# Performance work log

Hardware: AMD Instinct MI355X
Metric: run time of the kernel (lower is better)

Reference implementation:

```python
import jax, jax.numpy as jnp
import numpy as np

B, L, E, H = 4, 2048, 1024, 16
D = E // H  # per-head dim

def setup_inputs() -> dict:
    key = jax.random.key(0)
    ks = jax.random.split(key, 12)
    xav = lambda k, shape: jax.random.normal(k, shape, jnp.float32) * (2.0 / (shape[0] + shape[-1])) ** 0.5
    embeddings = jax.random.normal(ks[0], (B, L, E), jnp.float32)
    pre_proj_w = xav(ks[1], (E, E)); pre_proj_b = jnp.zeros((E,), jnp.float32)
    pre_sparse_w = xav(ks[2], (E, E)); pre_sparse_b = jnp.zeros((E,), jnp.float32)
    toeplitz_psfs = xav(ks[3], (H, 2 * L - 1, D))
    post_conv_w = xav(ks[4], (E, E)); post_conv_b = jnp.zeros((E,), jnp.float32)
    dens = 0.01
    num_nz = int(L * L * dens)
    idxs = jax.random.randint(ks[5], (num_nz, 2), 0, L)
    vals = jnp.abs(jax.random.normal(ks[6], (num_nz,), jnp.float32))
    sparse = jnp.zeros((L, L), jnp.float32).at[idxs[:, 0], idxs[:, 1]].add(vals)
    ln_gamma = jnp.ones((E,), jnp.float32); ln_beta = jnp.zeros((E,), jnp.float32)
    return {"embeddings": embeddings, "pre_proj_w": pre_proj_w, "pre_proj_b": pre_proj_b,
            "pre_sparse_w": pre_sparse_w, "pre_sparse_b": pre_sparse_b,
            "toeplitz_psfs": toeplitz_psfs, "post_conv_w": post_conv_w, "post_conv_b": post_conv_b,
            "sparse": sparse, "ln_gamma": ln_gamma, "ln_beta": ln_beta}

def reference(embeddings, pre_proj_w, pre_proj_b, pre_sparse_w, pre_sparse_b,
              toeplitz_psfs, post_conv_w, post_conv_b, sparse, ln_gamma, ln_beta):
    b, l, e = embeddings.shape
    h, two_l_m1, d = toeplitz_psfs.shape
    # causal PSF mask: first l taps kept, trailing l-1 zeroed (before softmax)
    psf_mask = jnp.concatenate([jnp.ones((l,)), jnp.zeros((l - 1,))])[None, :, None]
    psfs = jax.nn.softmax(toeplitz_psfs * psf_mask, axis=1)  # softmax over 2l-1 taps
    # pre-projection
    pre = jnp.einsum('ble,oe->blo', embeddings, pre_proj_w) + pre_proj_b
    # pad seq to 2l-1 and split heads: [b, h, 2l-1, d]
    padded = jnp.pad(pre, ((0, 0), (0, l - 1), (0, 0)))
    padded = padded.reshape(b, two_l_m1, h, d).transpose(0, 2, 1, 3)
    # 2D FFT convolution over (seq, per-head-dim)
    psf_fft = jnp.fft.fftn(psfs, axes=(1, 2))              # [h, 2l-1, d]
    emb_fft = jnp.fft.fftn(padded, axes=(2, 3))            # [b, h, 2l-1, d]
    conv = jnp.real(jnp.fft.ifftn(psf_fft[None] * emb_fft, axes=(2, 3)))[:, :, :l, :]
    conv = jax.nn.gelu(conv, approximate=False)
    conv = conv.transpose(0, 2, 1, 3).reshape(b, l, e)
    conv_emb = jnp.einsum('ble,oe->blo', conv, post_conv_w) + post_conv_b
    # sparse branch (causal lower-triangular mask)
    sparse_masked = sparse * jnp.tril(jnp.ones((l, l), sparse.dtype))
    pre_sparse = jnp.einsum('ble,oe->blo', pre, pre_sparse_w) + pre_sparse_b
    sparse_emb = jnp.einsum('ls,bse->ble', sparse_masked, pre_sparse)
    # residual + layernorm (dropout = identity at eval)
    x = conv_emb + sparse_emb + embeddings
    mu = jnp.mean(x, axis=-1, keepdims=True)
    var = jnp.mean(jnp.square(x - mu), axis=-1, keepdims=True)
    return (x - mu) * jax.lax.rsqrt(var + 1e-12) * ln_gamma + ln_beta
```

## Files before the change

### kernel.cpp

```cpp
#include <hip/hip_runtime.h>
#include <hip/hip_bf16.h>
#include <hip/hip_fp16.h>
#include <math.h>

#define B_ 4
#define L_ 2048
#define E_ 1024
#define H_ 16
#define D_ 64
#define NFFT 4096
#define CAP 128

typedef __hip_bfloat16 bf16;
typedef __attribute__((ext_vector_type(8))) short bf16x8;
typedef __attribute__((ext_vector_type(4))) float f32x4;
typedef __attribute__((ext_vector_type(2))) __fp16 f16x2;

typedef __attribute__((address_space(1))) const unsigned int gas_u32;
typedef __attribute__((address_space(3))) unsigned int las_u32;

__device__ __forceinline__ void gload_lds16(const void* g, void* l) {
    __builtin_amdgcn_global_load_lds((gas_u32*)g, (las_u32*)l, 16, 0, 0);
}

#define SL(i) ((i) + ((i) >> 4))
#define LDSN (NFFT + NFFT / 16)

__device__ __forceinline__ float bfu2f(unsigned short u) {
    return __uint_as_float(((unsigned)u) << 16);
}
__device__ __forceinline__ f16x2 pk2(float a, float b) {
    return __builtin_amdgcn_cvt_pkrtz(a, b);
}

__device__ __forceinline__ int drev64(int k) {
    return ((k & 3) << 4) | (k & 12) | ((k >> 4) & 3);
}

#define C1R 0.923879532511287f
#define C1I -0.382683432365090f
#define C2R 0.707106781186548f
#define C2I -0.707106781186548f
#define C3R 0.382683432365090f
#define C3I -0.923879532511287f

__device__ __forceinline__ void r4dif_w(float& x0r, float& x0i, float& x1r, float& x1i,
                                        float& x2r, float& x2i, float& x3r, float& x3i,
                                        float w1r, float w1i) {
    float a0r = x0r + x2r, a0i = x0i + x2i, a1r = x0r - x2r, a1i = x0i - x2i;
    float a2r = x1r + x3r, a2i = x1i + x3i, a3r = x1r - x3r, a3i = x1i - x3i;
    float y0r = a0r + a2r, y0i = a0i + a2i, y2r = a0r - a2r, y2i = a0i - a2i;
    float y1r = a1r + a3i, y1i = a1i - a3r, y3r = a1r - a3i, y3i = a1i + a3r;
    float w2r = w1r * w1r - w1i * w1i, w2i = 2.0f * w1r * w1i;
    float w3r = w2r * w1r - w2i * w1i, w3i = w2r * w1i + w2i * w1r;
    x0r = y0r; x0i = y0i;
    x1r = y1r * w1r - y1i * w1i; x1i = y1r * w1i + y1i * w1r;
    x2r = y2r * w2r - y2i * w2i; x2i = y2r * w2i + y2i * w2r;
    x3r = y3r * w3r - y3i * w3i; x3i = y3r * w3i + y3i * w3r;
}
__device__ __forceinline__ void r4dif_nt(float& x0r, float& x0i, float& x1r, float& x1i,
                                         float& x2r, float& x2i, float& x3r, float& x3i) {
    float a0r = x0r + x2r, a0i = x0i + x2i, a1r = x0r - x2r, a1i = x0i - x2i;
    float a2r = x1r + x3r, a2i = x1i + x3i, a3r = x1r - x3r, a3i = x1i - x3i;
    x0r = a0r + a2r; x0i = a0i + a2i;
    x2r = a0r - a2r; x2i = a0i - a2i;
    float y1r = a1r + a3i, y1i = a1i - a3r, y3r = a1r - a3i, y3i = a1i + a3r;
    x1r = y1r; x1i = y1i; x3r = y3r; x3i = y3i;
}
__device__ __forceinline__ void r4dit_w(float& x0r, float& x0i, float& x1r, float& x1i,
                                        float& x2r, float& x2i, float& x3r, float& x3i,
                                        float w1r, float w1i) {
    float w2r = w1r * w1r - w1i * w1i, w2i = 2.0f * w1r * w1i;
    float w3r = w2r * w1r - w2i * w1i, w3i = w2r * w1i + w2i * w1r;
    float z1r = x1r * w1r + x1i * w1i, z1i = x1i * w1r - x1r * w1i;
    float z2r = x2r * w2r + x2i * w2i, z2i = x2i * w2r - x2r * w2i;
    float z3r = x3r * w3r + x3i * w3i, z3i = x3i * w3r - x3r * w3i;
    float b0r = x0r + z2r, b0i = x0i + z2i, b1r = x0r - z2r, b1i = x0i - z2i;
    float b2r = z1r + z3r, b2i = z1i + z3i, b3r = z1r - z3r, b3i = z1i - z3i;
    x0r = b0r + b2r; x0i = b0i + b2i;
    x2r = b0r - b2r; x2i = b0i - b2i;
    x1r = b1r - b3i; x1i = b1i + b3r;
    x3r = b1r + b3i; x3i = b1i - b3r;
}
__device__ __forceinline__ void r4dit_nt(float& x0r, float& x0i, float& x1r, float& x1i,
                                         float& x2r, float& x2i, float& x3r, float& x3i) {
    float b0r = x0r + x2r, b0i = x0i + x2i, b1r = x0r - x2r, b1i = x0i - x2i;
    float b2r = x1r + x3r, b2i = x1i + x3i, b3r = x1r - x3r, b3i = x1i - x3i;
    x0r = b0r + b2r; x0i = b0i + b2i;
    x2r = b0r - b2r; x2i = b0i - b2i;
    x1r = b1r - b3i; x1i = b1i + b3r;
    x3r = b1r + b3i; x3i = b1i - b3r;
}

__device__ __forceinline__ void fftA_fwd(float* xr, float* xi, float wpr, float wpi) {
    r4dif_w(xr[0], xi[0], xr[4], xi[4], xr[8], xi[8], xr[12], xi[12], wpr, wpi);
    r4dif_w(xr[1], xi[1], xr[5], xi[5], xr[9], xi[9], xr[13], xi[13],
            wpr * C1R - wpi * C1I, wpr * C1I + wpi * C1R);
    r4dif_w(xr[2], xi[2], xr[6], xi[6], xr[10], xi[10], xr[14], xi[14],
            wpr * C2R - wpi * C2I, wpr * C2I + wpi * C2R);
    r4dif_w(xr[3], xi[3], xr[7], xi[7], xr[11], xi[11], xr[15], xi[15],
            wpr * C3R - wpi * C3I, wpr * C3I + wpi * C3R);
    float s2r = wpr * wpr - wpi * wpi, s2i = 2.0f * wpr * wpi;
    float w4r = s2r * s2r - s2i * s2i, w4i = 2.0f * s2r * s2i;
#pragma unroll
    for (int g = 0; g < 4; ++g)
        r4dif_w(xr[4 * g], xi[4 * g], xr[4 * g + 1], xi[4 * g + 1], xr[4 * g + 2],
                xi[4 * g + 2], xr[4 * g + 3], xi[4 * g + 3], w4r, w4i);
}
__device__ __forceinline__ void fftA_inv(float* xr, float* xi, float wpr, float wpi) {
    float s2r = wpr * wpr - wpi * wpi, s2i = 2.0f * wpr * wpi;
    float w4r = s2r * s2r - s2i * s2i, w4i = 2.0f * s2r * s2i;
#pragma unroll
    for (int g = 0; g < 4; ++g)
        r4dit_w(xr[4 * g], xi[4 * g], xr[4 * g + 1], xi[4 * g + 1], xr[4 * g + 2],
                xi[4 * g + 2], xr[4 * g + 3], xi[4 * g + 3], w4r, w4i);
    r4dit_w(xr[0], xi[0], xr[4], xi[4], xr[8], xi[8], xr[12], xi[12], wpr, wpi);
    r4dit_w(xr[1], xi[1], xr[5], xi[5], xr[9], xi[9], xr[13], xi[13],
            wpr * C1R - wpi * C1I, wpr * C1I + wpi * C1R);
    r4dit_w(xr[2], xi[2], xr[6], xi[6], xr[10], xi[10], xr[14], xi[14],
            wpr * C2R - wpi * C2I, wpr * C2I + wpi * C2R);
    r4dit_w(xr[3], xi[3], xr[7], xi[7], xr[11], xi[11], xr[15], xi[15],
            wpr * C3R - wpi * C3I, wpr * C3I + wpi * C3R);
}
__device__ __forceinline__ void fftB_fwd(float* xr, float* xi, float wor, float woi) {
    r4dif_w(xr[0], xi[0], xr[4], xi[4], xr[8], xi[8], xr[12], xi[12], wor, woi);
    r4dif_w(xr[1], xi[1], xr[5], xi[5], xr[9], xi[9], xr[13], xi[13],
            wor * C1R - woi * C1I, wor * C1I + woi * C1R);
    r4dif_w(xr[2], xi[2], xr[6], xi[6], xr[10], xi[10], xr[14], xi[14],
            wor * C2R - woi * C2I, wor * C2I + woi * C2R);
    r4dif_w(xr[3], xi[3], xr[7], xi[7], xr[11], xi[11], xr[15], xi[15],
            wor * C3R - woi * C3I, wor * C3I + woi * C3R);
    float s2r = wor * wor - woi * woi, s2i = 2.0f * wor * woi;
    float w4r = s2r * s2r - s2i * s2i, w4i = 2.0f * s2r * s2i;
#pragma unroll
    for (int g = 0; g < 4; ++g)
        r4dif_w(xr[4 * g], xi[4 * g], xr[4 * g + 1], xi[4 * g + 1], xr[4 * g + 2],
                xi[4 * g + 2], xr[4 * g + 3], xi[4 * g + 3], w4r, w4i);
}
__device__ __forceinline__ void fftB_inv(float* xr, float* xi, float wor, float woi) {
    float s2r = wor * wor - woi * woi, s2i = 2.0f * wor * woi;
    float w4r = s2r * s2r - s2i * s2i, w4i = 2.0f * s2r * s2i;
#pragma unroll
    for (int g = 0; g < 4; ++g)
        r4dit_w(xr[4 * g], xi[4 * g], xr[4 * g + 1], xi[4 * g + 1], xr[4 * g + 2],
                xi[4 * g + 2], xr[4 * g + 3], xi[4 * g + 3], w4r, w4i);
    r4dit_w(xr[0], xi[0], xr[4], xi[4], xr[8], xi[8], xr[12], xi[12], wor, woi);
    r4dit_w(xr[1], xi[1], xr[5], xi[5], xr[9], xi[9], xr[13], xi[13],
            wor * C1R - woi * C1I, wor * C1I + woi * C1R);
    r4dit_w(xr[2], xi[2], xr[6], xi[6], xr[10], xi[10], xr[14], xi[14],
            wor * C2R - woi * C2I, wor * C2I + woi * C2R);
    r4dit_w(xr[3], xi[3], xr[7], xi[7], xr[11], xi[11], xr[15], xi[15],
            wor * C3R - woi * C3I, wor * C3I + woi * C3R);
}
__device__ __forceinline__ void fftC_fwd(float* xr, float* xi) {
    r4dif_w(xr[0], xi[0], xr[4], xi[4], xr[8], xi[8], xr[12], xi[12], 1.0f, 0.0f);
    r4dif_w(xr[1], xi[1], xr[5], xi[5], xr[9], xi[9], xr[13], xi[13], C1R, C1I);
    r4dif_w(xr[2], xi[2], xr[6], xi[6], xr[10], xi[10], xr[14], xi[14], C2R, C2I);
    r4dif_w(xr[3], xi[3], xr[7], xi[7], xr[11], xi[11], xr[15], xi[15], C3R, C3I);
#pragma unroll
    for (int g = 0; g < 4; ++g)
        r4dif_nt(xr[4 * g], xi[4 * g], xr[4 * g + 1], xi[4 * g + 1], xr[4 * g + 2],
                 xi[4 * g + 2], xr[4 * g + 3], xi[4 * g + 3]);
}
__device__ __forceinline__ void fftC_inv(float* xr, float* xi) {
#pragma unroll
    for (int g = 0; g < 4; ++g)
        r4dit_nt(xr[4 * g], xi[4 * g], xr[4 * g + 1], xi[4 * g + 1], xr[4 * g + 2],
                 xi[4 * g + 2], xr[4 * g + 3], xi[4 * g + 3]);
    r4dit_w(xr[0], xi[0], xr[4], xi[4], xr[8], xi[8], xr[12], xi[12], 1.0f, 0.0f);
    r4dit_w(xr[1], xi[1], xr[5], xi[5], xr[9], xi[9], xr[13], xi[13], C1R, C1I);
    r4dit_w(xr[2], xi[2], xr[6], xi[6], xr[10], xi[10], xr[14], xi[14], C2R, C2I);
    r4dit_w(xr[3], xi[3], xr[7], xi[7], xr[11], xi[11], xr[15], xi[15], C3R, C3I);
}

template <int CONJ>
__device__ inline void fft64_rows(float* xr, float* xi, int tid,
                                  const float2* __restrict__ tw) {
    for (int st = 0; st < 3; ++st) {
        int q = 1 << (4 - 2 * st);
        __syncthreads();
        for (int it = 0; it < 4; ++it) {
            int w = tid + (it << 8);
            int lc = w & 63, bc = w >> 6;
            int p = bc & (q - 1);
            int basev = ((bc & ~(q - 1)) << 2) | p;
            int i0 = basev * 66 + lc, i1 = i0 + q * 66, i2 = i1 + q * 66, i3 = i2 + q * 66;
            float x0r = xr[i0], x0i = xi[i0], x1r = xr[i1], x1i = xi[i1];
            float x2r = xr[i2], x2i = xi[i2], x3r = xr[i3], x3i = xi[i3];
            float a0r = x0r + x2r, a0i = x0i + x2i;
            float a1r = x0r - x2r, a1i = x0i - x2i;
            float a2r = x1r + x3r, a2i = x1i + x3i;
            float a3r = x1r - x3r, a3i = x1i - x3i;
            float y0r = a0r + a2r, y0i = a0i + a2i;
            float y2r = a0r - a2r, y2i = a0i - a2i;
            float y1r, y1i, y3r, y3i;
            if (!CONJ) {
                y1r = a1r + a3i; y1i = a1i - a3r;
                y3r = a1r - a3i; y3i = a1i + a3r;
            } else {
                y1r = a1r - a3i; y1i = a1i + a3r;
                y3r = a1r + a3i; y3i = a1i - a3r;
            }
            int e = (p << (2 * st)) * 64;
            float2 w1 = tw[e];
            float w1x = w1.x, w1y = CONJ ? -w1.y : w1.y;
            float w2x = w1x * w1x - w1y * w1y, w2y = 2.0f * w1x * w1y;
            float w3x = w2x * w1x - w2y * w1y, w3y = w2x * w1y + w2y * w1x;
            xr[i0] = y0r; xi[i0] = y0i;
            xr[i1] = y1r * w1x - y1i * w1y; xi[i1] = y1r * w1y + y1i * w1x;
            xr[i2] = y2r * w2x - y2i * w2y; xi[i2] = y2r * w2y + y2i * w2x;
            xr[i3] = y3r * w3x - y3i * w3y; xi[i3] = y3r * w3y + y3i * w3x;
        }
    }
    __syncthreads();
}

__device__ inline void fft64_b(float* xr, float* xi, int tid,
                               const float2* __restrict__ tw) {
    for (int st = 0; st < 3; ++st) {
        int q = 1 << (4 - 2 * st);
        __syncthreads();
        for (int it = 0; it < 4; ++it) {
            int b = tid + (it << 8);
            int fc = b & 63;
            int bc = b >> 6;
            int p = bc & (q - 1);
            int basev = ((bc & ~(q - 1)) << 2) | p;
            int i0 = basev * 64 + fc, i1 = i0 + q * 64, i2 = i1 + q * 64, i3 = i2 + q * 64;
            float x0r = xr[i0], x0i = xi[i0], x1r = xr[i1], x1i = xi[i1];
            float x2r = xr[i2], x2i = xi[i2], x3r = xr[i3], x3i = xi[i3];
            float a0r = x0r + x2r, a0i = x0i + x2i;
            float a1r = x0r - x2r, a1i = x0i - x2i;
            float a2r = x1r + x3r, a2i = x1i + x3i;
            float a3r = x1r - x3r, a3i = x1i - x3i;
            float y0r = a0r + a2r, y0i = a0i + a2i;
            float y2r = a0r - a2r, y2i = a0i - a2i;
            float y1r = a1r + a3i, y1i = a1i - a3r;
            float y3r = a1r - a3i, y3i = a1i + a3r;
            int e = (p << (2 * st)) * 64;
            float2 w1 = tw[e];
            float w2x = w1.x * w1.x - w1.y * w1.y, w2y = 2.0f * w1.x * w1.y;
            float w3x = w2x * w1.x - w2y * w1.y, w3y = w2x * w1.y + w2y * w1.x;
            xr[i0] = y0r; xi[i0] = y0i;
            xr[i1] = y1r * w1.x - y1i * w1.y; xi[i1] = y1r * w1.y + y1i * w1.x;
            xr[i2] = y2r * w2x - y2i * w2y; xi[i2] = y2r * w2y + y2i * w2x;
            xr[i3] = y3r * w3x - y3i * w3y; xi[i3] = y3r * w3y + y3i * w3x;
        }
    }
    __syncthreads();
}

#define NB_TW 16
#define NB_CVT 8192
#define NB_CVTW 3072
#define NB_TF 512
#define NB_SP 2048
__global__ __launch_bounds__(256) void k_prologue(const float* __restrict__ emb,
                                                  const float* __restrict__ W1,
                                                  const float* __restrict__ W2,
                                                  const float* __restrict__ W3,
                                                  const float* __restrict__ psfs,
                                                  const float* __restrict__ Sp,
                                                  float2* __restrict__ tw,
                                                  bf16* __restrict__ embb,
                                                  bf16* __restrict__ Wb,
                                                  float* __restrict__ psfT,
                                                  int* __restrict__ nnz,
                                                  int* __restrict__ idxs,
                                                  float* __restrict__ vals) {
    __shared__ float tile[64][65];
    __shared__ int cnt;
    int tid = threadIdx.x;
    int blk = blockIdx.x;
    if (blk < NB_TW) {
        int k = blk * 256 + tid;
        float ang = -(float)k * (float)(M_PI / 2048.0);
        tw[k] = make_float2(cosf(ang), sinf(ang));
        return;
    }
    blk -= NB_TW;
    if (blk < NB_CVT) {
        int i = (blk * 256 + tid) * 4;
        float4 v = *(const float4*)(emb + i);
        bf16 tmp[4];
        tmp[0] = __float2bfloat16(v.x); tmp[1] = __float2bfloat16(v.y);
        tmp[2] = __float2bfloat16(v.z); tmp[3] = __float2bfloat16(v.w);
        *(ushort4*)(embb + i) = *(ushort4*)tmp;
        return;
    }
    blk -= NB_CVT;
    if (blk < NB_CVTW) {
        int w = blk >> 10;
        const float* src = (w == 0) ? W1 : (w == 1) ? W2 : W3;
        int i = ((blk & 1023) * 256 + tid) * 4;
        float4 v = *(const float4*)(src + i);
        bf16 tmp[4];
        tmp[0] = __float2bfloat16(v.x); tmp[1] = __float2bfloat16(v.y);
        tmp[2] = __float2bfloat16(v.z); tmp[3] = __float2bfloat16(v.w);
        *(ushort4*)(Wb + (size_t)w * E_ * E_ + i) = *(ushort4*)tmp;
        return;
    }
    blk -= NB_CVTW;
    if (blk < NB_TF) {
        int z = blk >> 5;
        int r0 = (blk & 31) * 64;
        const float* in = psfs + (size_t)z * (2 * L_ - 1) * D_;
        float* out = psfT + (size_t)z * D_ * L_;
        int tx4 = (tid & 15) * 4, ty = tid >> 4;
#pragma unroll
        for (int k = 0; k < 4; ++k) {
            int r = ty + 16 * k;
            float4 v = *(const float4*)&in[(size_t)(r0 + r) * D_ + tx4];
            tile[r][tx4 + 0] = v.x; tile[r][tx4 + 1] = v.y;
            tile[r][tx4 + 2] = v.z; tile[r][tx4 + 3] = v.w;
        }
        __syncthreads();
#pragma unroll
        for (int k = 0; k < 4; ++k) {
            int c = ty + 16 * k;
            float4 w;
            w.x = tile[tx4 + 0][c]; w.y = tile[tx4 + 1][c];
            w.z = tile[tx4 + 2][c]; w.w = tile[tx4 + 3][c];
            *(float4*)&out[(size_t)c * L_ + r0 + tx4] = w;
        }
        return;
    }
    blk -= NB_TF;
    {
        int l = blk;
        if (tid == 0) cnt = 0;
        __syncthreads();
        const float* row = Sp + (size_t)l * L_;
        for (int s = tid; s <= l; s += 256) {
            float v = row[s];
            if (v != 0.0f) {
                int slot = atomicAdd(&cnt, 1);
                if (slot < CAP) { idxs[l * CAP + slot] = s; vals[l * CAP + slot] = v; }
            }
        }
        __syncthreads();
        if (tid == 0) nnz[l] = min(cnt, CAP);
    }
}

template <int OUTB>
__global__ __launch_bounds__(256) void k_gemm_mfma(const bf16* __restrict__ A,
                                                   const bf16* __restrict__ Wt,
                                                   const float* __restrict__ bias,
                                                   float* __restrict__ C,
                                                   bf16* __restrict__ Cb,
                                                   int M, int N, int K) {
    __shared__ bf16 As[64 * 64];
    __shared__ bf16 Bs[128 * 64];
    int tid = threadIdx.x;
    int lane = tid & 63, w = tid >> 6;
    int wr = w >> 1, wc = w & 1;

    int nwg = gridDim.x * gridDim.y;
    int flat = blockIdx.y * gridDim.x + blockIdx.x;
    int cpx = nwg >> 3;
    int swz = (flat & 7) * cpx + (flat >> 3);
    int bx = (swz % gridDim.x) * 128;
    int by = (swz / gridDim.x) * 64;

    f32x4 zz = {0.0f, 0.0f, 0.0f, 0.0f};
    f32x4 acc[2][4];
#pragma unroll
    for (int m = 0; m < 2; ++m)
#pragma unroll
        for (int n = 0; n < 4; ++n) acc[m][n] = zz;

    int koff = (lane >> 4) * 8;
    int rsub = lane & 15;

    for (int k0 = 0; k0 < K; k0 += 64) {
#pragma unroll
        for (int i = 0; i < 2; ++i) {
            int c = tid + i * 256;
            int row = c >> 3;
            int kb = (c & 7) * 8;
            int kbs = kb ^ ((row & 7) << 3);
            gload_lds16(A + (size_t)(by + row) * K + k0 + kbs, &As[c * 8]);
        }
#pragma unroll
        for (int i = 0; i < 4; ++i) {
            int c = tid + i * 256;
            int row = c >> 3;
            int kb = (c & 7) * 8;
            int kbs = kb ^ ((row & 7) << 3);
            gload_lds16(Wt + (size_t)(bx + row) * K + k0 + kbs, &Bs[c * 8]);
        }
        __syncthreads();
#pragma unroll
        for (int half = 0; half < 2; ++half) {
            int ko = koff + half * 32;
            bf16x8 af[2], bfv[4];
#pragma unroll
            for (int m = 0; m < 2; ++m) {
                int R = wr * 32 + m * 16 + rsub;
                af[m] = *(const bf16x8*)&As[R * 64 + (ko ^ ((R & 7) << 3))];
            }
#pragma unroll
            for (int n = 0; n < 4; ++n) {
                int R = wc * 64 + n * 16 + rsub;
                bfv[n] = *(const bf16x8*)&Bs[R * 64 + (ko ^ ((R & 7) << 3))];
            }
#pragma unroll
            for (int m = 0; m < 2; ++m)
#pragma unroll
                for (int n = 0; n < 4; ++n)
                    acc[m][n] = __builtin_amdgcn_mfma_f32_16x16x32_bf16(af[m], bfv[n], acc[m][n], 0, 0, 0);
        }
        __syncthreads();
    }

    int cq = (lane >> 4) * 4;
    int cr = lane & 15;
#pragma unroll
    for (int m = 0; m < 2; ++m) {
        int row0 = by + wr * 32 + m * 16 + cq;
#pragma unroll
        for (int n = 0; n < 4; ++n) {
            int col = bx + wc * 64 + n * 16 + cr;
            float bv = bias[col];
#pragma unroll
            for (int j = 0; j < 4; ++j) {
                float v = acc[m][n][j] + bv;
                if constexpr (OUTB)
                    Cb[(size_t)(row0 + j) * N + col] = __float2bfloat16(v);
                else
                    C[(size_t)(row0 + j) * N + col] = v;
            }
        }
    }
}

__global__ __launch_bounds__(256) void k_build_khat(const float* __restrict__ psfT,
                                                    f16x2* __restrict__ Khat,
                                                    const float2* __restrict__ tw) {
    __shared__ f16x2 fl[LDSN];
    __shared__ float red[256];
    int u = blockIdx.x, h = blockIdx.y, tid = threadIdx.x;
    const float* col = psfT + ((size_t)(h * D_ + u)) * L_;
    int p = tid;

    float2 twp = tw[p];
    float2 two = tw[(tid & 15) * 16];

    float v[8];
#pragma unroll
    for (int j = 0; j < 8; ++j) v[j] = col[p + 256 * j];

    float lm = v[0];
#pragma unroll
    for (int j = 1; j < 8; ++j) lm = fmaxf(lm, v[j]);
    red[tid] = lm; __syncthreads();
    for (int off = 128; off > 0; off >>= 1) {
        if (tid < off) red[tid] = fmaxf(red[tid], red[tid + off]);
        __syncthreads();
    }
    float M = fmaxf(red[0], 0.0f);
    __syncthreads();

    float e[8];
    float ls = 0.0f;
#pragma unroll
    for (int j = 0; j < 8; ++j) { e[j] = expf(v[j] - M); ls += e[j]; }
    red[tid] = ls; __syncthreads();
    for (int off = 128; off > 0; off >>= 1) {
        if (tid < off) red[tid] += red[tid + off];
        __syncthreads();
    }
    float Z = red[0] + (float)(L_ - 1) * expf(-M);
    float invZ = 1.0f / Z;
    float cval = expf(-M) * invZ;

    float xr[16], xi[16];
#pragma unroll
    for (int j = 0; j < 16; ++j) {
        int i = p + 256 * j;
        xr[j] = (j < 8) ? e[j] * invZ : ((i == 2048) ? 0.0f : cval);
        xi[j] = 0.0f;
    }
    __syncthreads();

    fftA_fwd(xr, xi, twp.x, twp.y);
#pragma unroll
    for (int j = 0; j < 16; ++j) fl[SL(p + 256 * j)] = pk2(xr[j], xi[j]);
    __syncthreads();
    {
        int bb = tid >> 4, o = tid & 15;
#pragma unroll
        for (int j = 0; j < 16; ++j) {
            f16x2 hh = fl[SL(bb * 256 + o + 16 * j)];
            xr[j] = (float)hh.x; xi[j] = (float)hh.y;
        }
        fftB_fwd(xr, xi, two.x, two.y);
#pragma unroll
        for (int j = 0; j < 16; ++j)
            fl[SL(bb * 256 + o + 16 * j)] = pk2(xr[j], xi[j]);
    }
    __syncthreads();
#pragma unroll
    for (int j = 0; j < 16; ++j) {
        f16x2 hh = fl[SL(16 * tid + j)];
        xr[j] = (float)hh.x; xi[j] = (float)hh.y;
    }
    fftC_fwd(xr, xi);

    float sc = 1.0f / (float)NFFT;
    f16x2* outp = Khat + ((size_t)h * D_ + u) * NFFT + 16 * tid;
#pragma unroll
    for (int j = 0; j < 16; ++j) outp[j] = pk2(xr[j] * sc, xi[j] * sc);
}

__global__ __launch_bounds__(256) void k_dfft_vfft(f16x2* __restrict__ Khat,
                                                   const bf16* __restrict__ preb,
                                                   f16x2* __restrict__ Xv,
                                                   const float2* __restrict__ tw) {
    __shared__ float smem[2 * 4224];
    float* Xre = smem;
    float* Xim = smem + 4224;
    int tid = threadIdx.x;
    int blk = blockIdx.x;
    if (blk < 1024) {
        int f0 = (blk & 63) * 64, h = blk >> 6;
        f16x2* kb = Khat + (size_t)h * D_ * NFFT;
        for (int i = tid; i < 4096; i += 256) {
            int uu = i >> 6, fc = i & 63;
            f16x2 v = kb[(size_t)uu * NFFT + f0 + fc];
            Xre[i] = (float)v.x; Xim[i] = (float)v.y;
        }
        fft64_b(Xre, Xim, tid, tw);
        float sc = 1.0f / 64.0f;
        for (int i = tid; i < 4096; i += 256) {
            int s = i >> 6, fc = i & 63;
            kb[(size_t)drev64(s) * NFFT + f0 + fc] = pk2(Xre[i] * sc, Xim[i] * sc);
        }
        return;
    }
    blk -= 1024;
    {
        int l0 = (blk & 31) * 64, h = (blk >> 5) & 15, b = blk >> 9;
        const bf16* src = preb + ((size_t)(b * L_ + l0)) * E_ + h * 64;
#pragma unroll
        for (int it = 0; it < 2; ++it) {
            int c = tid + it * 256;
            int lc = c >> 3, v8 = (c & 7) * 8;
            bf16x8 xv8 = *(const bf16x8*)(src + (size_t)lc * E_ + v8);
#pragma unroll
            for (int j = 0; j < 8; ++j) {
                Xre[(v8 + j) * 66 + lc] = bfu2f((unsigned short)xv8[j]);
                Xim[(v8 + j) * 66 + lc] = 0.0f;
            }
        }
        fft64_rows<0>(Xre, Xim, tid, tw);
        for (int i = tid; i < 33 * 64; i += 256) {
            int k = i >> 6, lc = i & 63;
            int s = drev64(k);
            Xv[((size_t)(b * H_ + h) * 33 + k) * L_ + l0 + lc] =
                pk2(Xre[s * 66 + lc], Xim[s * 66 + lc]);
        }
    }
}

__global__ __launch_bounds__(256) void k_seqconv(f16x2* __restrict__ Xv,
                                                 const f16x2* __restrict__ Khat,
                                                 const float2* __restrict__ tw) {
    __shared__ f16x2 fl[LDSN];
    int k = blockIdx.x, h = blockIdx.y, b = blockIdx.z;
    int tid = threadIdx.x, p = tid;
    f16x2* col = Xv + ((size_t)(b * H_ + h) * 33 + k) * L_;

    float2 twp = tw[p];
    float2 two = tw[(tid & 15) * 16];

    float xr[16], xi[16];
#pragma unroll
    for (int j = 0; j < 16; ++j) {
        if (j < 8) {
            f16x2 z = col[p + 256 * j];
            xr[j] = (float)z.x; xi[j] = (float)z.y;
        } else { xr[j] = 0.0f; xi[j] = 0.0f; }
    }
    fftA_fwd(xr, xi, twp.x, twp.y);
#pragma unroll
    for (int j = 0; j < 16; ++j) fl[SL(p + 256 * j)] = pk2(xr[j], xi[j]);
    __syncthreads();
    {
        int bb = tid >> 4, o = tid & 15;
#pragma unroll
        for (int j = 0; j < 16; ++j) {
            f16x2 hh = fl[SL(bb * 256 + o + 16 * j)];
            xr[j] = (float)hh.x; xi[j] = (float)hh.y;
        }
        fftB_fwd(xr, xi, two.x, two.y);
#pragma unroll
        for (int j = 0; j < 16; ++j)
            fl[SL(bb * 256 + o + 16 * j)] = pk2(xr[j], xi[j]);
    }
    __syncthreads();
    {
        const f16x2* khp = Khat + ((size_t)h * 64 + k) * NFFT + 16 * tid;
        f16x2 kk[16];
#pragma unroll
        for (int j = 0; j < 16; ++j) kk[j] = khp[j];
#pragma unroll
        for (int j = 0; j < 16; ++j) {
            f16x2 hh = fl[SL(16 * tid + j)];
            xr[j] = (float)hh.x; xi[j] = (float)hh.y;
        }
        fftC_fwd(xr, xi);
#pragma unroll
        for (int j = 0; j < 16; ++j) {
            float kr = (float)kk[j].x, ki = (float)kk[j].y;
            float ar = xr[j], ai = xi[j];
            xr[j] = ar * kr - ai * ki;
            xi[j] = ar * ki + ai * kr;
        }
        fftC_inv(xr, xi);
#pragma unroll
        for (int j = 0; j < 16; ++j) fl[SL(16 * tid + j)] = pk2(xr[j], xi[j]);
    }
    __syncthreads();
    {
        int bb = tid >> 4, o = tid & 15;
#pragma unroll
        for (int j = 0; j < 16; ++j) {
            f16x2 hh = fl[SL(bb * 256 + o + 16 * j)];
            xr[j] = (float)hh.x; xi[j] = (float)hh.y;
        }
        fftB_inv(xr, xi, two.x, two.y);
#pragma unroll
        for (int j = 0; j < 16; ++j)
            fl[SL(bb * 256 + o + 16 * j)] = pk2(xr[j], xi[j]);
    }
    __syncthreads();
#pragma unroll
    for (int j = 0; j < 16; ++j) {
        f16x2 hh = fl[SL(p + 256 * j)];
        xr[j] = (float)hh.x; xi[j] = (float)hh.y;
    }
    fftA_inv(xr, xi, twp.x, twp.y);
#pragma unroll
    for (int j = 0; j < 8; ++j)
        col[p + 256 * j] = pk2(xr[j], xi[j]);
}

__global__ __launch_bounds__(256) void k_vifft(const f16x2* __restrict__ Xv,
                                               bf16* __restrict__ actb,
                                               const float2* __restrict__ tw) {
    __shared__ float Xre[64 * 66];
    __shared__ float Xim[64 * 66];
    int l0 = blockIdx.x * 64, h = blockIdx.y, b = blockIdx.z;
    int tid = threadIdx.x;
    for (int i = tid; i < 33 * 64; i += 256) {
        int k = i >> 6, lc = i & 63;
        f16x2 z = Xv[((size_t)(b * H_ + h) * 33 + k) * L_ + l0 + lc];
        Xre[k * 66 + lc] = (float)z.x; Xim[k * 66 + lc] = (float)z.y;
    }
    __syncthreads();
    for (int i = tid; i < 31 * 64; i += 256) {
        int k = 33 + (i >> 6), lc = i & 63;
        Xre[k * 66 + lc] =  Xre[(64 - k) * 66 + lc];
        Xim[k * 66 + lc] = -Xim[(64 - k) * 66 + lc];
    }
    fft64_rows<1>(Xre, Xim, tid, tw);
    bf16* dst = actb + ((size_t)(b * L_ + l0)) * E_ + h * 64;
#pragma unroll
    for (int it = 0; it < 2; ++it) {
        int c = tid + it * 256;
        int lc = c >> 3, m8 = (c & 7) * 8;
        unsigned short o[8];
#pragma unroll
        for (int j = 0; j < 8; ++j) {
            float x = Xre[drev64(m8 + j) * 66 + lc];
            float g = 0.5f * x * (1.0f + erff(x * 0.70710678118654752f));
            bf16 bb = __float2bfloat16(g);
            o[j] = *(unsigned short*)&bb;
        }
        *(ushort4*)(dst + (size_t)lc * E_ + m8)     = make_ushort4(o[0], o[1], o[2], o[3]);
        *(ushort4*)(dst + (size_t)lc * E_ + m8 + 4) = make_ushort4(o[4], o[5], o[6], o[7]);
    }
}

__global__ __launch_bounds__(256) void k_spmm_ln(const int* __restrict__ nnz,
                                                 const int* __restrict__ idxs,
                                                 const float* __restrict__ vals,
                                                 const bf16* __restrict__ P,
                                                 const bf16* __restrict__ accbb,
                                                 const float* __restrict__ emb,
                                                 const float* __restrict__ gamma,
                                                 const float* __restrict__ beta,
                                                 float* __restrict__ outp) {
    __shared__ int sidx[CAP];
    __shared__ float sval[CAP];
    __shared__ float red[256];
    int l = blockIdx.x, b = blockIdx.y, tid = threadIdx.x;
    int n = nnz[l];
    for (int j = tid; j < n; j += 256) {
        sidx[j] = idxs[l * CAP + j];
        sval[j] = vals[l * CAP + j];
    }
    __syncthreads();
    size_t off = (size_t)tid * 4;
    size_t rowbase = ((size_t)(b * L_ + l)) * E_;
    ushort4 a4 = *(const ushort4*)(accbb + rowbase + off);
    float4 e4 = *(const float4*)(emb + rowbase + off);
    float x0 = bfu2f(a4.x) + e4.x;
    float x1 = bfu2f(a4.y) + e4.y;
    float x2 = bfu2f(a4.z) + e4.z;
    float x3 = bfu2f(a4.w) + e4.w;
    const bf16* Pb = P + (size_t)b * L_ * E_;
    for (int j = 0; j < n; ++j) {
        float v = sval[j];
        ushort4 p = *(const ushort4*)(Pb + (size_t)sidx[j] * E_ + off);
        x0 += v * bfu2f(p.x); x1 += v * bfu2f(p.y);
        x2 += v * bfu2f(p.z); x3 += v * bfu2f(p.w);
    }
    red[tid] = x0 + x1 + x2 + x3; __syncthreads();
    for (int o2 = 128; o2 > 0; o2 >>= 1) {
        if (tid < o2) red[tid] += red[tid + o2];
        __syncthreads();
    }
    float mu = red[0] * (1.0f / E_);
    __syncthreads();
    float d0 = x0 - mu, d1 = x1 - mu, d2 = x2 - mu, d3 = x3 - mu;
    red[tid] = d0 * d0 + d1 * d1 + d2 * d2 + d3 * d3; __syncthreads();
    for (int o2 = 128; o2 > 0; o2 >>= 1) {
        if (tid < o2) red[tid] += red[tid + o2];
        __syncthreads();
    }
    float inv = rsqrtf(red[0] * (1.0f / E_) + 1e-12f);
    float4 g4 = *(const float4*)(gamma + off);
    float4 b4 = *(const float4*)(beta + off);
    float4 o4;
    o4.x = d0 * inv * g4.x + b4.x;
    o4.y = d1 * inv * g4.y + b4.y;
    o4.z = d2 * inv * g4.z + b4.z;
    o4.w = d3 * inv * g4.w + b4.w;
    *(float4*)(outp + rowbase + off) = o4;
}

extern "C" void kernel_launch(void* const* d_in, const int* in_sizes, int n_in,
                              void* d_out, int out_size, void* d_ws, size_t ws_size,
                              hipStream_t stream) {
    const float* emb    = (const float*)d_in[0];
    const float* W1     = (const float*)d_in[1];
    const float* b1     = (const float*)d_in[2];
    const float* W2     = (const float*)d_in[3];
    const float* b2     = (const float*)d_in[4];
    const float* psfs   = (const float*)d_in[5];
    const float* W3     = (const float*)d_in[6];
    const float* b3     = (const float*)d_in[7];
    const float* sparse = (const float*)d_in[8];
    const float* gamma  = (const float*)d_in[9];
    const float* beta   = (const float*)d_in[10];
    float* outp = (float*)d_out;

    const size_t BLE  = (size_t)B_ * L_ * E_;
    const size_t EE   = (size_t)E_ * E_;
    const size_t KSZ  = (size_t)H_ * D_ * NFFT;
    const size_t XVSZ = (size_t)B_ * H_ * 33 * L_;

    bf16*   accbb      = (bf16*)d_ws;
    bf16*   pre_sparse = accbb + BLE;
    f16x2*  Khat       = (f16x2*)(pre_sparse + BLE);
    f16x2*  Xv         = Khat + KSZ;
    bf16*   preb       = (bf16*)(Xv + XVSZ);
    bf16*   actb       = preb + BLE;
    bf16*   W1b        = actb + BLE;
    bf16*   W2b        = W1b + EE;
    bf16*   W3b        = W2b + EE;
    float2* twd        = (float2*)(W3b + EE);
    int*    s_nnz      = (int*)(twd + NFFT);
    int*    s_idx      = s_nnz + L_;
    float*  s_val      = (float*)(s_idx + (size_t)L_ * CAP);
    float*  psfT       = (float*)Xv;

    k_prologue<<<NB_TW + NB_CVT + NB_CVTW + NB_TF + NB_SP, 256, 0, stream>>>(
        emb, W1, W2, W3, psfs, sparse, twd, actb, W1b, psfT, s_nnz, s_idx, s_val);

    k_gemm_mfma<1><<<dim3(E_ / 128, (B_ * L_) / 64), 256, 0, stream>>>(
        actb, W1b, b1, nullptr, preb, B_ * L_, E_, E_);
    k_gemm_mfma<1><<<dim3(E_ / 128, (B_ * L_) / 64), 256, 0, stream>>>(
        preb, W2b, b2, nullptr, pre_sparse, B_ * L_, E_, E_);

    k_build_khat<<<dim3(D_, H_), 256, 0, stream>>>(psfT, Khat, twd);

    k_dfft_vfft<<<1024 + 2048, 256, 0, stream>>>(Khat, preb, Xv, twd);

    k_seqconv<<<dim3(33, H_, B_), 256, 0, stream>>>(Xv, Khat, twd);

    k_vifft<<<dim3(L_ / 64, H_, B_), 256, 0, stream>>>(Xv, actb, twd);

    k_gemm_mfma<1><<<dim3(E_ / 128, (B_ * L_) / 64), 256, 0, stream>>>(
        actb, W3b, b3, nullptr, accbb, B_ * L_, E_, E_);

    k_spmm_ln<<<dim3(L_, B_), 256, 0, stream>>>(
        s_nnz, s_idx, s_val, pre_sparse, accbb, emb, gamma, beta, outp);
}
```

Before: 210.5 us.

## Merge independent GEMM and FFT stages into shared heterogeneous launches

Packs independent work into combined kernels split by block index. The first GEMM now runs alongside the PSF kernel-FFT build, and the second GEMM runs alongside the D-axis FFT of Khat and the value FFT. The goal is to cut launch count and idle tail time by filling the GPU with independent work. The cost is that every block in a merged kernel reserves the largest shared-memory footprint (33 KB), which may lower occupancy for the GEMM blocks.

```diff
diff --git a/kernel.cpp b/kernel.cpp
--- a/kernel.cpp
+++ b/kernel.cpp
@@ -343,25 +343,22 @@
     }
 }
 
-template <int OUTB>
-__global__ __launch_bounds__(256) void k_gemm_mfma(const bf16* __restrict__ A,
-                                                   const bf16* __restrict__ Wt,
-                                                   const float* __restrict__ bias,
-                                                   float* __restrict__ C,
-                                                   bf16* __restrict__ Cb,
-                                                   int M, int N, int K) {
-    __shared__ bf16 As[64 * 64];
-    __shared__ bf16 Bs[128 * 64];
+__device__ __forceinline__ void gemm_body(void* smemraw, int flat, int nwgx,
+                                          const bf16* __restrict__ A,
+                                          const bf16* __restrict__ Wt,
+                                          const float* __restrict__ bias,
+                                          bf16* __restrict__ Cb,
+                                          int nwg, int N, int K) {
+    bf16* As = (bf16*)smemraw;
+    bf16* Bs = As + 64 * 64;
     int tid = threadIdx.x;
     int lane = tid & 63, w = tid >> 6;
     int wr = w >> 1, wc = w & 1;
 
-    int nwg = gridDim.x * gridDim.y;
-    int flat = blockIdx.y * gridDim.x + blockIdx.x;
     int cpx = nwg >> 3;
     int swz = (flat & 7) * cpx + (flat >> 3);
-    int bx = (swz % gridDim.x) * 128;
-    int by = (swz / gridDim.x) * 64;
+    int bx = (swz % nwgx) * 128;
+    int by = (swz / nwgx) * 64;
 
     f32x4 zz = {0.0f, 0.0f, 0.0f, 0.0f};
     f32x4 acc[2][4];
@@ -426,21 +423,20 @@
 #pragma unroll
             for (int j = 0; j < 4; ++j) {
                 float v = acc[m][n][j] + bv;
-                if constexpr (OUTB)
-                    Cb[(size_t)(row0 + j) * N + col] = __float2bfloat16(v);
-                else
-                    C[(size_t)(row0 + j) * N + col] = v;
+                Cb[(size_t)(row0 + j) * N + col] = __float2bfloat16(v);
             }
         }
     }
 }
 
-__global__ __launch_bounds__(256) void k_build_khat(const float* __restrict__ psfT,
-                                                    f16x2* __restrict__ Khat,
-                                                    const float2* __restrict__ tw) {
-    __shared__ f16x2 fl[LDSN];
-    __shared__ float red[256];
-    int u = blockIdx.x, h = blockIdx.y, tid = threadIdx.x;
+__device__ __forceinline__ void khat_body(void* smemraw, int blk,
+                                          const float* __restrict__ psfT,
+                                          f16x2* __restrict__ Khat,
+                                          const float2* __restrict__ tw) {
+    f16x2* fl = (f16x2*)smemraw;
+    float* red = (float*)(fl + LDSN);
+    int u = blk & 63, h = blk >> 6;
+    int tid = threadIdx.x;
     const float* col = psfT + ((size_t)(h * D_ + u)) * L_;
     int p = tid;
 
@@ -514,54 +510,94 @@
     for (int j = 0; j < 16; ++j) outp[j] = pk2(xr[j] * sc, xi[j] * sc);
 }
 
-__global__ __launch_bounds__(256) void k_dfft_vfft(f16x2* __restrict__ Khat,
-                                                   const bf16* __restrict__ preb,
-                                                   f16x2* __restrict__ Xv,
-                                                   const float2* __restrict__ tw) {
-    __shared__ float smem[2 * 4224];
-    float* Xre = smem;
-    float* Xim = smem + 4224;
+__device__ __forceinline__ void dfft_body(void* smemraw, int blk,
+                                          f16x2* __restrict__ Khat,
+                                          const float2* __restrict__ tw) {
+    float* Xre = (float*)smemraw;
+    float* Xim = Xre + 4224;
     int tid = threadIdx.x;
+    int f0 = (blk & 63) * 64, h = blk >> 6;
+    f16x2* kb = Khat + (size_t)h * D_ * NFFT;
+    for (int i = tid; i < 4096; i += 256) {
+        int uu = i >> 6, fc = i & 63;
+        f16x2 v = kb[(size_t)uu * NFFT + f0 + fc];
+        Xre[i] = (float)v.x; Xim[i] = (float)v.y;
+    }
+    fft64_b(Xre, Xim, tid, tw);
+    float sc = 1.0f / 64.0f;
+    for (int i = tid; i < 4096; i += 256) {
+        int s = i >> 6, fc = i & 63;
+        kb[(size_t)drev64(s) * NFFT + f0 + fc] = pk2(Xre[i] * sc, Xim[i] * sc);
+    }
+}
+
+__device__ __forceinline__ void vfft_body(void* smemraw, int blk,
+                                          const bf16* __restrict__ preb,
+                                          f16x2* __restrict__ Xv,
+                                          const float2* __restrict__ tw) {
+    float* Xre = (float*)smemraw;
+    float* Xim = Xre + 4224;
+    int tid = threadIdx.x;
+    int l0 = (blk & 31) * 64, h = (blk >> 5) & 15, b = blk >> 9;
+    const bf16* src = preb + ((size_t)(b * L_ + l0)) * E_ + h * 64;
+#pragma unroll
+    for (int it = 0; it < 2; ++it) {
+        int c = tid + it * 256;
+        int lc = c >> 3, v8 = (c & 7) * 8;
+        bf16x8 xv8 = *(const bf16x8*)(src + (size_t)lc * E_ + v8);
+#pragma unroll
+        for (int j = 0; j < 8; ++j) {
+            Xre[(v8 + j) * 66 + lc] = bfu2f((unsigned short)xv8[j]);
+            Xim[(v8 + j) * 66 + lc] = 0.0f;
+        }
+    }
+    fft64_rows<0>(Xre, Xim, tid, tw);
+    for (int i = tid; i < 33 * 64; i += 256) {
+        int k = i >> 6, lc = i & 63;
+        int s = drev64(k);
+        Xv[((size_t)(b * H_ + h) * 33 + k) * L_ + l0 + lc] =
+            pk2(Xre[s * 66 + lc], Xim[s * 66 + lc]);
+    }
+}
+
+__global__ __launch_bounds__(256) void k_gemm1_khat(const bf16* __restrict__ A,
+                                                    const bf16* __restrict__ Wt,
+                                                    const float* __restrict__ bias,
+                                                    bf16* __restrict__ Cb,
+                                                    const float* __restrict__ psfT,
+                                                    f16x2* __restrict__ Khat,
+                                                    const float2* __restrict__ tw) {
+    __shared__ __align__(16) char smem[24576];
     int blk = blockIdx.x;
-    if (blk < 1024) {
-        int f0 = (blk & 63) * 64, h = blk >> 6;
-        f16x2* kb = Khat + (size_t)h * D_ * NFFT;
-        for (int i = tid; i < 4096; i += 256) {
-            int uu = i >> 6, fc = i & 63;
-            f16x2 v = kb[(size_t)uu * NFFT + f0 + fc];
-            Xre[i] = (float)v.x; Xim[i] = (float)v.y;
-        }
-        fft64_b(Xre, Xim, tid, tw);
-        float sc = 1.0f / 64.0f;
-        for (int i = tid; i < 4096; i += 256) {
-            int s = i >> 6, fc = i & 63;
-            kb[(size_t)drev64(s) * NFFT + f0 + fc] = pk2(Xre[i] * sc, Xim[i] * sc);
-        }
-        return;
-    }
-    blk -= 1024;
-    {
-        int l0 = (blk & 31) * 64, h = (blk >> 5) & 15, b = blk >> 9;
-        const bf16* src = preb + ((size_t)(b * L_ + l0)) * E_ + h * 64;
-#pragma unroll
-        for (int it = 0; it < 2; ++it) {
-            int c = tid + it * 256;
-            int lc = c >> 3, v8 = (c & 7) * 8;
-            bf16x8 xv8 = *(const bf16x8*)(src + (size_t)lc * E_ + v8);
-#pragma unroll
-            for (int j = 0; j < 8; ++j) {
-                Xre[(v8 + j) * 66 + lc] = bfu2f((unsigned short)xv8[j]);
-                Xim[(v8 + j) * 66 + lc] = 0.0f;
-            }
-        }
-        fft64_rows<0>(Xre, Xim, tid, tw);
-        for (int i = tid; i < 33 * 64; i += 256) {
-            int k = i >> 6, lc = i & 63;
-            int s = drev64(k);
-            Xv[((size_t)(b * H_ + h) * 33 + k) * L_ + l0 + lc] =
-                pk2(Xre[s * 66 + lc], Xim[s * 66 + lc]);
-        }
-    }
+    if (blk < 1024)
+        gemm_body(smem, blk, 8, A, Wt, bias, Cb, 1024, E_, E_);
+    else
+        khat_body(smem, blk - 1024, psfT, Khat, tw);
+}
+
+__global__ __launch_bounds__(256) void k_gemm2_dfft_vfft(const bf16* __restrict__ A,
+                                                         const bf16* __restrict__ Wt,
+                                                         const float* __restrict__ bias,
+                                                         bf16* __restrict__ Cb,
+                                                         f16x2* __restrict__ Khat,
+                                                         f16x2* __restrict__ Xv,
+                                                         const float2* __restrict__ tw) {
+    __shared__ __align__(16) char smem[33792];
+    int blk = blockIdx.x;
+    if (blk < 1024)
+        gemm_body(smem, blk, 8, A, Wt, bias, Cb, 1024, E_, E_);
+    else if (blk < 2048)
+        dfft_body(smem, blk - 1024, Khat, tw);
+    else
+        vfft_body(smem, blk - 2048, A, Xv, tw);
+}
+
+__global__ __launch_bounds__(256) void k_gemm3(const bf16* __restrict__ A,
+                                               const bf16* __restrict__ Wt,
+                                               const float* __restrict__ bias,
+                                               bf16* __restrict__ Cb) {
+    __shared__ __align__(16) char smem[24576];
+    gemm_body(smem, blockIdx.x, 8, A, Wt, bias, Cb, 1024, E_, E_);
 }
 
 __global__ __launch_bounds__(256) void k_seqconv(f16x2* __restrict__ Xv,
@@ -781,21 +817,15 @@
     k_prologue<<<NB_TW + NB_CVT + NB_CVTW + NB_TF + NB_SP, 256, 0, stream>>>(
         emb, W1, W2, W3, psfs, sparse, twd, actb, W1b, psfT, s_nnz, s_idx, s_val);
 
-    k_gemm_mfma<1><<<dim3(E_ / 128, (B_ * L_) / 64), 256, 0, stream>>>(
-        actb, W1b, b1, nullptr, preb, B_ * L_, E_, E_);
-    k_gemm_mfma<1><<<dim3(E_ / 128, (B_ * L_) / 64), 256, 0, stream>>>(
-        preb, W2b, b2, nullptr, pre_sparse, B_ * L_, E_, E_);
-
-    k_build_khat<<<dim3(D_, H_), 256, 0, stream>>>(psfT, Khat, twd);
-
-    k_dfft_vfft<<<1024 + 2048, 256, 0, stream>>>(Khat, preb, Xv, twd);
+    k_gemm1_khat<<<2048, 256, 0, stream>>>(actb, W1b, b1, preb, psfT, Khat, twd);
+
+    k_gemm2_dfft_vfft<<<4096, 256, 0, stream>>>(preb, W2b, b2, pre_sparse, Khat, Xv, twd);
 
     k_seqconv<<<dim3(33, H_, B_), 256, 0, stream>>>(Xv, Khat, twd);
 
     k_vifft<<<dim3(L_ / 64, H_, B_), 256, 0, stream>>>(Xv, actb, twd);
 
-    k_gemm_mfma<1><<<dim3(E_ / 128, (B_ * L_) / 64), 256, 0, stream>>>(
-        actb, W3b, b3, nullptr, accbb, B_ * L_, E_, E_);
+    k_gemm3<<<1024, 256, 0, stream>>>(actb, W3b, b3, accbb);
 
     k_spmm_ln<<<dim3(L_, B_), 256, 0, stream>>>(
         s_nnz, s_idx, s_val, pre_sparse, accbb, emb, gamma, beta, outp);
```

Result: faster. 197.0 us, median of 3 (-6.4%).
